# Kernel optimization log

Hardware: AMD Instinct MI355X
Metric: run time of the kernel (lower is better)

The kernel has to match this reference:

```python
import jax, jax.numpy as jnp
import numpy as np

H = 4      # num_heads
D = 256    # hidden_dim
HD = 64    # head_dim
SCALE = HD ** -0.5


def setup_inputs() -> dict:
    key = jax.random.key(0)
    ks = jax.random.split(key, 5)
    x = jax.random.normal(ks[0], (4, 4096, D), dtype=jnp.float32)
    # Linear weights stored torch-style as [out, in]; y = x @ W.T
    init = 1.0 / np.sqrt(D)
    Wq = jax.random.uniform(ks[1], (D, D), jnp.float32, -init, init)
    Wk = jax.random.uniform(ks[2], (D, D), jnp.float32, -init, init)
    Wv = jax.random.uniform(ks[3], (D, D), jnp.float32, -init, init)
    Wo = jax.random.uniform(ks[4], (D, D), jnp.float32, -init, init)
    return {"x": x, "Wq": Wq, "Wk": Wk, "Wv": Wv, "Wo": Wo}


def reference(x, Wq, Wk, Wv, Wo):
    B, S, _ = x.shape
    # projections (torch Linear: x @ W.T)
    q = (x @ Wq.T).reshape(B, S, H, HD).transpose(0, 2, 1, 3)  # [B,H,S,HD]
    k = (x @ Wk.T).reshape(B, S, H, HD).transpose(0, 2, 1, 3)
    v = (x @ Wv.T).reshape(B, S, H, HD).transpose(0, 2, 1, 3)
    scores = jnp.einsum('bhqd,bhkd->bhqk', q, k) * SCALE  # [B,H,S,S]
    causal = jnp.triu(jnp.ones((S, S), dtype=bool), k=1)
    scores = jnp.where(causal[None, None], -jnp.inf, scores)
    attn = jax.nn.softmax(scores, axis=-1)
    out = jnp.einsum('bhqk,bhkd->bhqd', attn, v)  # [B,H,S,HD]
    out = out.transpose(0, 2, 1, 3).reshape(B, S, D)
    return out @ Wo.T
```

## Files before the change

kernel.cpp:

```cpp
#include <hip/hip_runtime.h>
#include <hip/hip_bf16.h>
#include <cstdint>

using short8  = __attribute__((ext_vector_type(8))) short;
using u16x8   = __attribute__((ext_vector_type(8))) unsigned short;
using u16x4   = __attribute__((ext_vector_type(4))) unsigned short;
using f32x4   = __attribute__((ext_vector_type(4))) float;
using f32x16  = __attribute__((ext_vector_type(16))) float;

constexpr int BN = 4, HN = 4, SN = 4096, DN = 256, HD = 64;
constexpr int MROWS = BN * SN;
constexpr float QSCL = 0.18033688011112042f;

__device__ __forceinline__ unsigned short f2bf(float x) {
  union { float f; unsigned int u; } c; c.f = x;
  unsigned int u = c.u;
  return (unsigned short)((u + 0x7fffu + ((u >> 16) & 1u)) >> 16);
}
__device__ __forceinline__ unsigned int cvt_pk_bf16(float a, float b) {
  unsigned int r;
  asm("v_cvt_pk_bf16_f32 %0, %1, %2" : "=v"(r) : "v"(a), "v"(b));
  return r;
}
__device__ __forceinline__ void pl32swap(unsigned int& a, unsigned int& b) {
  asm volatile("v_permlane32_swap_b32 %0, %1" : "+v"(a), "+v"(b));
}

#define GLDS16(g, l)                                                  \
  __builtin_amdgcn_global_load_lds(                                   \
      (const __attribute__((address_space(1))) void*)(g),             \
      (__attribute__((address_space(3))) void*)(l), 16, 0, 0)

__global__ __launch_bounds__(256) void convert_kernel(
    const float* __restrict__ x,  const float* __restrict__ Wq,
    const float* __restrict__ Wk, const float* __restrict__ Wv,
    const float* __restrict__ Wo,
    unsigned short* __restrict__ xb, unsigned short* __restrict__ Wcat,
    unsigned short* __restrict__ Wob) {
  const long NX4 = (long)MROWS * DN / 4;
  const long NW4 = 65536 / 4;
  const long total = NX4 + 4 * NW4;
  for (long i = (long)blockIdx.x * 256 + threadIdx.x; i < total;
       i += (long)gridDim.x * 256) {
    const float* src; unsigned short* dst;
    if (i < NX4) { src = x + i * 4; dst = xb + i * 4; }
    else {
      long j = i - NX4; int w = (int)(j >> 14); long o = (j & 16383) * 4;
      src = (w == 0 ? Wq : w == 1 ? Wk : w == 2 ? Wv : Wo) + o;
      dst = (w < 3 ? Wcat + (long)w * 65536 : Wob) + o;
    }
    float4 v = *(const float4*)src;
    u16x4 pk; pk[0] = f2bf(v.x); pk[1] = f2bf(v.y);
    pk[2] = f2bf(v.z); pk[3] = f2bf(v.w);
    *(u16x4*)dst = pk;
  }
}

template <int MODE, int NBN>
__global__ __launch_bounds__(256) void gemm_kernel(
    const unsigned short* __restrict__ Abf,
    const unsigned short* __restrict__ Bbf,
    unsigned short* __restrict__ qo, unsigned short* __restrict__ ko,
    unsigned short* __restrict__ vo, float* __restrict__ out) {
  constexpr int SMEM = (MODE == 1) ? 128 * 132 * 4 : 128 * 136 * 2;
  __shared__ __align__(16) char smem[SMEM];
  unsigned short* stg = (unsigned short*)smem;

  const int tid = threadIdx.x, lane = tid & 63, wid = tid >> 6;
  const int lo = lane & 15, hi = lane >> 4;
  const int bn = blockIdx.x % NBN, bm = blockIdx.x / NBN;
  const int wm = (wid >> 1) * 64, wn = (wid & 1) * 64;
  const long arow0 = (long)bm * 128, brow0 = (long)bn * 128;

  auto stage = [&](int buf, int kt) {
    const int row = (wid * 2) * 16 + (lane >> 2);
    const int col = (lane & 3) * 8;
    const unsigned short* ga = Abf + (arow0 + row) * DN + kt * 32 + col;
    const unsigned short* gb = Bbf + (brow0 + row) * DN + kt * 32 + col;
    unsigned short* la = stg + buf * 8192 + wid * 1024;
    unsigned short* lb = la + 4096;
    GLDS16(ga, la);
    GLDS16(ga + 16 * DN, la + 512);
    GLDS16(gb, lb);
    GLDS16(gb + 16 * DN, lb + 512);
  };

  f32x4 acc[4][4];
#pragma unroll
  for (int a = 0; a < 4; ++a)
#pragma unroll
    for (int b = 0; b < 4; ++b)
#pragma unroll
      for (int e = 0; e < 4; ++e) acc[a][b][e] = 0.f;

  stage(0, 0);
#pragma unroll
  for (int kt = 0; kt < 8; ++kt) {
    const int buf = kt & 1;
    __syncthreads();
    if (kt < 7) stage(buf ^ 1, kt + 1);
    const unsigned short* sa = stg + buf * 8192;
    const unsigned short* sb = sa + 4096;
    short8 af[4], bf[4];
#pragma unroll
    for (int f = 0; f < 4; ++f) {
      af[f] = *(const short8*)(sa + (wm + f * 16 + lo) * 32 + hi * 8);
      bf[f] = *(const short8*)(sb + (wn + f * 16 + lo) * 32 + hi * 8);
    }
#pragma unroll
    for (int fn = 0; fn < 4; ++fn)
#pragma unroll
      for (int fm = 0; fm < 4; ++fm)
        acc[fn][fm] = __builtin_amdgcn_mfma_f32_16x16x32_bf16(
            bf[fn], af[fm], acc[fn][fm], 0, 0, 0);
  }
  __syncthreads();

  if constexpr (MODE == 0) {
    unsigned short* cs = (unsigned short*)smem;
    if (bn < 4) {
      const float cscl = (bn < 2) ? QSCL : 1.0f;
#pragma unroll
      for (int fn = 0; fn < 4; ++fn)
#pragma unroll
        for (int fm = 0; fm < 4; ++fm) {
          u16x4 pk;
#pragma unroll
          for (int r = 0; r < 4; ++r) pk[r] = f2bf(acc[fn][fm][r] * cscl);
          const int m = wm + fm * 16 + lo, n0 = wn + fn * 16 + hi * 4;
          *(u16x4*)(cs + m * 136 + n0) = pk;
        }
      __syncthreads();
      unsigned short* dstmat = (bn < 2) ? qo : ko;
      const int colbase = (bn & 1) * 128;
#pragma unroll
      for (int p = 0; p < 8; ++p) {
        const int ml = p * 16 + (tid >> 4), n0 = (tid & 15) * 8;
        u16x8 v = *(u16x8*)(cs + ml * 136 + n0);
        const int c = colbase + n0, h = c >> 6, hd = c & 63;
        const long m = arow0 + ml;
        const int b = (int)(m >> 12), s = (int)(m & 4095);
        *(u16x8*)(dstmat + ((long)(b * HN + h) * SN + s) * HD + hd) = v;
      }
    } else {
#pragma unroll
      for (int fn = 0; fn < 4; ++fn)
#pragma unroll
        for (int fm = 0; fm < 4; ++fm) {
          const int m = wm + fm * 16 + lo, n0 = wn + fn * 16 + hi * 4;
#pragma unroll
          for (int r = 0; r < 4; ++r)
            cs[(n0 + r) * 136 + m] = f2bf(acc[fn][fm][r]);
        }
      __syncthreads();
      const int b = (int)(arow0 >> 12), sbase = (int)(arow0 & 4095);
#pragma unroll
      for (int p = 0; p < 8; ++p) {
        const int cl = p * 16 + (tid >> 4);
        const int s0 = (tid & 15) * 8;
        u16x8 v = *(u16x8*)(cs + cl * 136 + s0);
        const int c = (bn & 1) * 128 + cl, h = c >> 6, hd = c & 63;
        *(u16x8*)(vo + ((long)((b * HN + h) * HD + hd)) * SN + sbase + s0) = v;
      }
    }
  } else {
    float* csf = (float*)smem;
#pragma unroll
    for (int fn = 0; fn < 4; ++fn)
#pragma unroll
      for (int fm = 0; fm < 4; ++fm) {
        const int m = wm + fm * 16 + lo, n0 = wn + fn * 16 + hi * 4;
        *(f32x4*)(csf + m * 132 + n0) = acc[fn][fm];
      }
    __syncthreads();
#pragma unroll
    for (int p = 0; p < 8; ++p) {
      const int ml = p * 16 + (tid >> 4), n0 = (tid & 15) * 8;
      f32x4 v0 = *(f32x4*)(csf + ml * 132 + n0);
      f32x4 v1 = *(f32x4*)(csf + ml * 132 + n0 + 4);
      float* dst = out + (arow0 + ml) * DN + bn * 128 + n0;
      *(f32x4*)dst = v0;
      *(f32x4*)(dst + 4) = v1;
    }
  }
}

template <int NSPLIT>
__global__ __launch_bounds__(256, 2) void attn_kernel(
    const unsigned short* __restrict__ Qw, const unsigned short* __restrict__ Kw,
    const unsigned short* __restrict__ VTp, unsigned short* __restrict__ Ow,
    float* __restrict__ Op, float* __restrict__ Mp, float* __restrict__ Lp) {
  __shared__ __align__(16) unsigned short sK[2][4096];
  __shared__ __align__(16) unsigned short sV[2][4096];

  const int tid = threadIdx.x;
  const int w = tid >> 6, lane = tid & 63;
  const int l31 = lane & 31, h5 = lane >> 5;
  const int bid = blockIdx.x;
  const int bh = (bid & 7) * 2 + ((bid >> 3) & 1);
  int c, g;
  if constexpr (NSPLIT == 4)      { c = (bid >> 4) & 3; g = bid >> 6; }
  else if constexpr (NSPLIT == 2) { c = (bid >> 4) & 1; g = bid >> 5; }
  else                            { c = 0;             g = bid >> 4; }
  const int t = 31 - g;
  const int q0 = t * 128;
  const int qw = q0 + w * 32;
  const long base = (long)bh * SN * HD;
  const int tlast = 2 * t + 1;
  const int wlast = 2 * t + (w >> 1);

  const int sr = w * 16 + (lane >> 3);
  const int gcol8 = (((lane & 7) ^ (lane >> 3)) << 3);
  auto stage = [&](int buf, int k0) {
    const unsigned short* gk = Kw + base + (long)(k0 + sr) * HD + gcol8;
    GLDS16(gk, &sK[buf][w * 1024]);
    GLDS16(gk + 8 * HD, &sK[buf][w * 1024 + 512]);
    const unsigned short* gv = VTp + base + (long)sr * SN + k0 + gcol8;
    GLDS16(gv, &sV[buf][w * 1024]);
    GLDS16(gv + 8 * SN, &sV[buf][w * 1024 + 512]);
  };

  short8 qf[4];
#pragma unroll
  for (int ks = 0; ks < 4; ++ks)
    qf[ks] = *(const short8*)(Qw + base + (long)(qw + l31) * HD + ks * 16 + h5 * 8);

  f32x16 oacc[2];
#pragma unroll
  for (int oh = 0; oh < 2; ++oh)
#pragma unroll
    for (int r = 0; r < 16; ++r) oacc[oh][r] = 0.f;
  float m_ = -INFINITY, l_ = 0.f;

  const int swz = (l31 & 7) << 3;

  stage(0, c * 64);
  __syncthreads();
  int buf = 0;
  for (int kt = c; kt <= tlast; kt += NSPLIT) {
    if (kt + NSPLIT <= tlast) stage(buf ^ 1, (kt + NSPLIT) * 64);

    if (kt <= wlast) {
      const int k0 = kt * 64;
      short8 kb[8];
#pragma unroll
      for (int s = 0; s < 2; ++s)
#pragma unroll
        for (int ks = 0; ks < 4; ++ks)
          kb[s * 4 + ks] = *(const short8*)&sK[buf][(32 * s + l31) * 64 +
                                                   (((2 * ks + h5) << 3) ^ swz)];
      f32x16 c0, c1;
#pragma unroll
      for (int r = 0; r < 16; ++r) { c0[r] = 0.f; c1[r] = 0.f; }
#pragma unroll
      for (int ks = 0; ks < 4; ++ks)
        c0 = __builtin_amdgcn_mfma_f32_32x32x16_bf16(kb[ks], qf[ks], c0, 0, 0, 0);
#pragma unroll
      for (int ks = 0; ks < 4; ++ks)
        c1 = __builtin_amdgcn_mfma_f32_32x32x16_bf16(kb[4 + ks], qf[ks], c1, 0, 0, 0);

      short8 vt0[4], vt1[4];
#pragma unroll
      for (int ks = 0; ks < 4; ++ks) {
        const int col = ((2 * ks + h5) << 3) ^ swz;
        vt0[ks] = *(const short8*)&sV[buf][l31 * 64 + col];
        vt1[ks] = *(const short8*)&sV[buf][(32 + l31) * 64 + col];
      }

      if (kt == wlast) {
        const int mb0 = k0 + 4 * h5 - qw - l31;
#pragma unroll
        for (int r = 0; r < 16; ++r) {
          const int d = (r & 3) + 8 * (r >> 2);
          if (mb0 + d > 0)      c0[r] = -INFINITY;
          if (mb0 + 32 + d > 0) c1[r] = -INFINITY;
        }
      }

      float mv[16];
#pragma unroll
      for (int r = 0; r < 16; ++r) mv[r] = fmaxf(c0[r], c1[r]);
#pragma unroll
      for (int st = 8; st >= 1; st >>= 1)
#pragma unroll
        for (int i = 0; i < st; ++i) mv[i] = fmaxf(mv[i], mv[i + st]);
      const float mx = fmaxf(mv[0], __shfl_xor(mv[0], 32, 64));

      if (__any(mx > m_ + 11.5f)) {
        const float mn = fmaxf(m_, mx);
        const float alpha = __builtin_amdgcn_exp2f(m_ - mn);
        m_ = mn;
        l_ *= alpha;
#pragma unroll
        for (int oh = 0; oh < 2; ++oh)
#pragma unroll
          for (int r = 0; r < 16; ++r) oacc[oh][r] *= alpha;
      }

#pragma unroll
      for (int r = 0; r < 16; ++r) {
        c0[r] = __builtin_amdgcn_exp2f(c0[r] - m_);
        c1[r] = __builtin_amdgcn_exp2f(c1[r] - m_);
      }
      float sv[16];
#pragma unroll
      for (int r = 0; r < 16; ++r) sv[r] = c0[r] + c1[r];
#pragma unroll
      for (int st = 8; st >= 1; st >>= 1)
#pragma unroll
        for (int i = 0; i < st; ++i) sv[i] += sv[i + st];
      l_ += sv[0] + __shfl_xor(sv[0], 32, 64);

      short8 pb[4];
#pragma unroll
      for (int s = 0; s < 2; ++s)
#pragma unroll
        for (int u = 0; u < 2; ++u) {
          unsigned int a0, a1, b0, b1;
          if (s == 0) {
            a0 = cvt_pk_bf16(c0[8 * u + 0], c0[8 * u + 1]);
            a1 = cvt_pk_bf16(c0[8 * u + 2], c0[8 * u + 3]);
            b0 = cvt_pk_bf16(c0[8 * u + 4], c0[8 * u + 5]);
            b1 = cvt_pk_bf16(c0[8 * u + 6], c0[8 * u + 7]);
          } else {
            a0 = cvt_pk_bf16(c1[8 * u + 0], c1[8 * u + 1]);
            a1 = cvt_pk_bf16(c1[8 * u + 2], c1[8 * u + 3]);
            b0 = cvt_pk_bf16(c1[8 * u + 4], c1[8 * u + 5]);
            b1 = cvt_pk_bf16(c1[8 * u + 6], c1[8 * u + 7]);
          }
          pl32swap(a0, b0);
          pl32swap(a1, b1);
          union { unsigned int u4[4]; short8 v; } pu;
          pu.u4[0] = a0; pu.u4[1] = a1; pu.u4[2] = b0; pu.u4[3] = b1;
          pb[s * 2 + u] = pu.v;
        }

#pragma unroll
      for (int ks = 0; ks < 4; ++ks) {
        oacc[0] = __builtin_amdgcn_mfma_f32_32x32x16_bf16(vt0[ks], pb[ks], oacc[0], 0, 0, 0);
        oacc[1] = __builtin_amdgcn_mfma_f32_32x32x16_bf16(vt1[ks], pb[ks], oacc[1], 0, 0, 0);
      }
    }

    __syncthreads();
    buf ^= 1;
  }

  if constexpr (NSPLIT == 1) {
    unsigned short* ob = (unsigned short*)sK;
    const float rl = 1.f / l_;
#pragma unroll
    for (int oh = 0; oh < 2; ++oh)
#pragma unroll
      for (int rq = 0; rq < 4; ++rq) {
        const int hdb = 32 * oh + 8 * rq + 4 * h5;
        const unsigned int u0 = cvt_pk_bf16(oacc[oh][4 * rq + 0] * rl,
                                            oacc[oh][4 * rq + 1] * rl);
        const unsigned int u1 = cvt_pk_bf16(oacc[oh][4 * rq + 2] * rl,
                                            oacc[oh][4 * rq + 3] * rl);
        *(uint2*)&ob[w * 2048 + l31 * 64 + (hdb ^ ((l31 & 7) << 3))] =
            make_uint2(u0, u1);
      }
    __syncthreads();
    const int b = bh >> 2, h = bh & 3;
#pragma unroll
    for (int pass = 0; pass < 4; ++pass) {
      const int idx = pass * 256 + tid;
      const int row = idx >> 3, j = idx & 7;
      const int wreg = row >> 5, qi = row & 31;
      u16x8 vv = *(u16x8*)&ob[wreg * 2048 + qi * 64 +
                              ((j * 8) ^ ((qi & 7) << 3))];
      *(u16x8*)(Ow + ((long)(b * SN + q0 + row)) * DN + h * HD + j * 8) = vv;
    }
  } else {
    const long pb0 = (long)(c * 16 + bh) * 64;
#pragma unroll
    for (int oh = 0; oh < 2; ++oh)
#pragma unroll
      for (int rq = 0; rq < 4; ++rq)
#pragma unroll
        for (int e = 0; e < 4; ++e) {
          const int hd = 32 * oh + 8 * rq + 4 * h5 + e;
          Op[(pb0 + hd) * SN + qw + l31] = oacc[oh][4 * rq + e];
        }
    if (h5 == 0) {
      Mp[(long)(c * 16 + bh) * SN + qw + l31] = m_;
      Lp[(long)(c * 16 + bh) * SN + qw + l31] = l_;
    }
  }
}

template <int NS>
__global__ __launch_bounds__(256) void merge_kernel(
    const float* __restrict__ Op, const float* __restrict__ Mp,
    const float* __restrict__ Lp, unsigned short* __restrict__ Ow) {
  __shared__ float wsm[NS][64];
  __shared__ __align__(16) unsigned short obuf[64][72];
  const int tid = threadIdx.x;
  const int bh = blockIdx.x >> 6;
  const int qb = (blockIdx.x & 63) * 64;
  if (tid < 64) {
    const int q = qb + tid;
    float m[NS], l[NS];
    float ms = -INFINITY;
#pragma unroll
    for (int i = 0; i < NS; ++i) {
      m[i] = Mp[(long)(i * 16 + bh) * SN + q];
      l[i] = Lp[(long)(i * 16 + bh) * SN + q];
      ms = fmaxf(ms, m[i]);
    }
    float denom = 0.f, a[NS];
#pragma unroll
    for (int i = 0; i < NS; ++i) {
      a[i] = __builtin_amdgcn_exp2f(m[i] - ms);
      denom += l[i] * a[i];
    }
    const float rl = 1.f / denom;
#pragma unroll
    for (int i = 0; i < NS; ++i) wsm[i][tid] = a[i] * rl;
  }
  __syncthreads();
#pragma unroll
  for (int pass = 0; pass < 16; ++pass) {
    const int idx = pass * 256 + tid;
    const int hd = idx >> 6, q = idx & 63;
    float acc = 0.f;
#pragma unroll
    for (int i = 0; i < NS; ++i)
      acc += Op[((long)(i * 16 + bh) * 64 + hd) * SN + qb + q] * wsm[i][q];
    obuf[q][hd ^ ((q & 7) << 3)] = f2bf(acc);
  }
  __syncthreads();
  const int b = bh >> 2, h = bh & 3;
#pragma unroll
  for (int pass = 0; pass < 4; ++pass) {
    const int idx = pass * 256 + tid;
    const int q = idx >> 4, hg = (idx & 15) * 4;
    uint2 v = *(uint2*)&obuf[q][hg ^ ((q & 7) << 3)];
    *(uint2*)(Ow + ((long)(b * SN + qb + q)) * DN + h * HD + hg) = v;
  }
}

extern "C" void kernel_launch(void* const* d_in, const int* in_sizes, int n_in,
                              void* d_out, int out_size, void* d_ws, size_t ws_size,
                              hipStream_t stream) {
  const float* x  = (const float*)d_in[0];
  const float* Wq = (const float*)d_in[1];
  const float* Wk = (const float*)d_in[2];
  const float* Wv = (const float*)d_in[3];
  const float* Wo = (const float*)d_in[4];
  float* out = (float*)d_out;

  const size_t per = (size_t)MROWS * DN;
  unsigned short* xb   = (unsigned short*)d_ws;
  unsigned short* Wcat = xb + per;
  unsigned short* Wob  = Wcat + 768 * 256;
  unsigned short* Qw   = Wob + 65536;
  unsigned short* Kw   = Qw + per;
  unsigned short* VTw  = Kw + per;
  unsigned short* Ow   = xb;
  const size_t base_bytes = (4 * per + 768 * 256 + 65536) * sizeof(unsigned short);
  float* Op = (float*)((char*)d_ws + base_bytes);
  auto need = [&](int ns) {
    return base_bytes +
        ((size_t)ns * 16 * 64 * SN + 2 * (size_t)ns * 16 * SN) * sizeof(float);
  };

  convert_kernel<<<2048, 256, 0, stream>>>(x, Wq, Wk, Wv, Wo, xb, Wcat, Wob);
  gemm_kernel<0, 6><<<6 * (MROWS / 128), 256, 0, stream>>>(
      xb, Wcat, Qw, Kw, VTw, nullptr);
  if (ws_size >= need(4)) {
    float* Mp = Op + (size_t)4 * 16 * 64 * SN;
    float* Lp = Mp + (size_t)4 * 16 * SN;
    attn_kernel<4><<<2048, 256, 0, stream>>>(Qw, Kw, VTw, nullptr, Op, Mp, Lp);
    merge_kernel<4><<<16 * (SN / 64), 256, 0, stream>>>(Op, Mp, Lp, Ow);
  } else if (ws_size >= need(2)) {
    float* Mp = Op + (size_t)2 * 16 * 64 * SN;
    float* Lp = Mp + (size_t)2 * 16 * SN;
    attn_kernel<2><<<1024, 256, 0, stream>>>(Qw, Kw, VTw, nullptr, Op, Mp, Lp);
    merge_kernel<2><<<16 * (SN / 64), 256, 0, stream>>>(Op, Mp, Lp, Ow);
  } else {
    attn_kernel<1><<<512, 256, 0, stream>>>(
        Qw, Kw, VTw, Ow, nullptr, nullptr, nullptr);
  }
  gemm_kernel<1, 2><<<2 * (MROWS / 128), 256, 0, stream>>>(
      Ow, Wob, nullptr, nullptr, nullptr, out);
}
```

Before: 102.8 us.

## Use 512-thread attention blocks over 256-row query tiles with 2-way KV split

The attention kernel moves from 256-thread blocks over 128 query rows to 512-thread blocks over 256 query rows. Each staged K/V tile is now shared by eight waves, and each wave loads one row group instead of two. Query tiles are ordered to pair long and short causal tiles, and the split count drops from four to two, which cuts partial-output traffic and merge work. In exchange there are fewer blocks, each wave has a longer serial loop, and causal load balance across blocks is coarser. The first QK MFMA now accumulates into a zero vector rather than clearing the accumulators in a separate loop.

```diff
diff --git a/kernel.cpp b/kernel.cpp
--- a/kernel.cpp
+++ b/kernel.cpp
@@ -186,12 +186,11 @@
 }
 
 template <int NSPLIT>
-__global__ __launch_bounds__(256, 2) void attn_kernel(
+__global__ __launch_bounds__(512, 4) void attn_kernel(
     const unsigned short* __restrict__ Qw, const unsigned short* __restrict__ Kw,
     const unsigned short* __restrict__ VTp, unsigned short* __restrict__ Ow,
     float* __restrict__ Op, float* __restrict__ Mp, float* __restrict__ Lp) {
-  __shared__ __align__(16) unsigned short sK[2][4096];
-  __shared__ __align__(16) unsigned short sV[2][4096];
+  __shared__ __align__(16) unsigned short sMem[2][8192];
 
   const int tid = threadIdx.x;
   const int w = tid >> 6, lane = tid & 63;
@@ -199,25 +198,22 @@
   const int bid = blockIdx.x;
   const int bh = (bid & 7) * 2 + ((bid >> 3) & 1);
   int c, g;
-  if constexpr (NSPLIT == 4)      { c = (bid >> 4) & 3; g = bid >> 6; }
-  else if constexpr (NSPLIT == 2) { c = (bid >> 4) & 1; g = bid >> 5; }
-  else                            { c = 0;             g = bid >> 4; }
-  const int t = 31 - g;
-  const int q0 = t * 128;
+  if constexpr (NSPLIT == 2) { c = (bid >> 4) & 1; g = bid >> 5; }
+  else { c = 0; g = bid >> 4; }
+  const int t = (g < 8) ? (15 - g) : (g - 8);
+  const int q0 = t * 256;
   const int qw = q0 + w * 32;
   const long base = (long)bh * SN * HD;
-  const int tlast = 2 * t + 1;
-  const int wlast = 2 * t + (w >> 1);
-
-  const int sr = w * 16 + (lane >> 3);
+  const int tlast = 4 * t + 3;
+  const int wlast = 4 * t + (w >> 1);
+
+  const int sr = w * 8 + (lane >> 3);
   const int gcol8 = (((lane & 7) ^ (lane >> 3)) << 3);
   auto stage = [&](int buf, int k0) {
     const unsigned short* gk = Kw + base + (long)(k0 + sr) * HD + gcol8;
-    GLDS16(gk, &sK[buf][w * 1024]);
-    GLDS16(gk + 8 * HD, &sK[buf][w * 1024 + 512]);
+    GLDS16(gk, &sMem[buf][w * 512]);
     const unsigned short* gv = VTp + base + (long)sr * SN + k0 + gcol8;
-    GLDS16(gv, &sV[buf][w * 1024]);
-    GLDS16(gv + 8 * SN, &sV[buf][w * 1024 + 512]);
+    GLDS16(gv, &sMem[buf][4096 + w * 512]);
   };
 
   short8 qf[4];
@@ -226,10 +222,10 @@
     qf[ks] = *(const short8*)(Qw + base + (long)(qw + l31) * HD + ks * 16 + h5 * 8);
 
   f32x16 oacc[2];
-#pragma unroll
-  for (int oh = 0; oh < 2; ++oh)
-#pragma unroll
-    for (int r = 0; r < 16; ++r) oacc[oh][r] = 0.f;
+  f32x16 zro;
+#pragma unroll
+  for (int r = 0; r < 16; ++r) zro[r] = 0.f;
+  oacc[0] = zro; oacc[1] = zro;
   float m_ = -INFINITY, l_ = 0.f;
 
   const int swz = (l31 & 7) << 3;
@@ -242,29 +238,31 @@
 
     if (kt <= wlast) {
       const int k0 = kt * 64;
+      const unsigned short* sK = &sMem[buf][0];
+      const unsigned short* sV = &sMem[buf][4096];
       short8 kb[8];
 #pragma unroll
       for (int s = 0; s < 2; ++s)
 #pragma unroll
         for (int ks = 0; ks < 4; ++ks)
-          kb[s * 4 + ks] = *(const short8*)&sK[buf][(32 * s + l31) * 64 +
-                                                   (((2 * ks + h5) << 3) ^ swz)];
+          kb[s * 4 + ks] = *(const short8*)&sK[(32 * s + l31) * 64 +
+                                              (((2 * ks + h5) << 3) ^ swz)];
       f32x16 c0, c1;
-#pragma unroll
-      for (int r = 0; r < 16; ++r) { c0[r] = 0.f; c1[r] = 0.f; }
-#pragma unroll
-      for (int ks = 0; ks < 4; ++ks)
+      c0 = __builtin_amdgcn_mfma_f32_32x32x16_bf16(kb[0], qf[0], zro, 0, 0, 0);
+      c1 = __builtin_amdgcn_mfma_f32_32x32x16_bf16(kb[4], qf[0], zro, 0, 0, 0);
+#pragma unroll
+      for (int ks = 1; ks < 4; ++ks)
         c0 = __builtin_amdgcn_mfma_f32_32x32x16_bf16(kb[ks], qf[ks], c0, 0, 0, 0);
 #pragma unroll
-      for (int ks = 0; ks < 4; ++ks)
+      for (int ks = 1; ks < 4; ++ks)
         c1 = __builtin_amdgcn_mfma_f32_32x32x16_bf16(kb[4 + ks], qf[ks], c1, 0, 0, 0);
 
       short8 vt0[4], vt1[4];
 #pragma unroll
       for (int ks = 0; ks < 4; ++ks) {
         const int col = ((2 * ks + h5) << 3) ^ swz;
-        vt0[ks] = *(const short8*)&sV[buf][l31 * 64 + col];
-        vt1[ks] = *(const short8*)&sV[buf][(32 + l31) * 64 + col];
+        vt0[ks] = *(const short8*)&sV[l31 * 64 + col];
+        vt1[ks] = *(const short8*)&sV[(32 + l31) * 64 + col];
       }
 
       if (kt == wlast) {
@@ -347,7 +345,7 @@
   }
 
   if constexpr (NSPLIT == 1) {
-    unsigned short* ob = (unsigned short*)sK;
+    unsigned short* ob = &sMem[0][0];
     const float rl = 1.f / l_;
 #pragma unroll
     for (int oh = 0; oh < 2; ++oh)
@@ -365,7 +363,7 @@
     const int b = bh >> 2, h = bh & 3;
 #pragma unroll
     for (int pass = 0; pass < 4; ++pass) {
-      const int idx = pass * 256 + tid;
+      const int idx = pass * 512 + tid;
       const int row = idx >> 3, j = idx & 7;
       const int wreg = row >> 5, qi = row & 31;
       u16x8 vv = *(u16x8*)&ob[wreg * 2048 + qi * 64 +
@@ -461,26 +459,19 @@
   unsigned short* Ow   = xb;
   const size_t base_bytes = (4 * per + 768 * 256 + 65536) * sizeof(unsigned short);
   float* Op = (float*)((char*)d_ws + base_bytes);
-  auto need = [&](int ns) {
-    return base_bytes +
-        ((size_t)ns * 16 * 64 * SN + 2 * (size_t)ns * 16 * SN) * sizeof(float);
-  };
+  float* Mp = Op + (size_t)2 * 16 * 64 * SN;
+  float* Lp = Mp + (size_t)2 * 16 * SN;
+  const size_t need = base_bytes +
+      ((size_t)2 * 16 * 64 * SN + 2 * (size_t)2 * 16 * SN) * sizeof(float);
 
   convert_kernel<<<2048, 256, 0, stream>>>(x, Wq, Wk, Wv, Wo, xb, Wcat, Wob);
   gemm_kernel<0, 6><<<6 * (MROWS / 128), 256, 0, stream>>>(
       xb, Wcat, Qw, Kw, VTw, nullptr);
-  if (ws_size >= need(4)) {
-    float* Mp = Op + (size_t)4 * 16 * 64 * SN;
-    float* Lp = Mp + (size_t)4 * 16 * SN;
-    attn_kernel<4><<<2048, 256, 0, stream>>>(Qw, Kw, VTw, nullptr, Op, Mp, Lp);
-    merge_kernel<4><<<16 * (SN / 64), 256, 0, stream>>>(Op, Mp, Lp, Ow);
-  } else if (ws_size >= need(2)) {
-    float* Mp = Op + (size_t)2 * 16 * 64 * SN;
-    float* Lp = Mp + (size_t)2 * 16 * SN;
-    attn_kernel<2><<<1024, 256, 0, stream>>>(Qw, Kw, VTw, nullptr, Op, Mp, Lp);
+  if (ws_size >= need) {
+    attn_kernel<2><<<512, 512, 0, stream>>>(Qw, Kw, VTw, nullptr, Op, Mp, Lp);
     merge_kernel<2><<<16 * (SN / 64), 256, 0, stream>>>(Op, Mp, Lp, Ow);
   } else {
-    attn_kernel<1><<<512, 256, 0, stream>>>(
+    attn_kernel<1><<<256, 512, 0, stream>>>(
         Qw, Kw, VTw, Ow, nullptr, nullptr, nullptr);
   }
   gemm_kernel<1, 2><<<2 * (MROWS / 128), 256, 0, stream>>>(
```

New measurement: 129.0 us. 1.26x slower.
